# Optimization experiments

Measured on AMD Instinct MI355X. Metric: run time of the kernel, lower is better.

The kernel has to match this reference:

```python
import jax, jax.numpy as jnp
import numpy as np

B, L = 64, 512
CONTACT_P = 0.03  # realistic sparse contact density

def setup_inputs() -> dict:
    key = jax.random.key(0)
    k1, k2, k3 = jax.random.split(key, 3)
    inputs = jax.random.normal(k1, (B, L, L), dtype=jnp.float32)
    targets = (jax.random.uniform(k2, (B, L, L)) < CONTACT_P).astype(jnp.float32)
    seq_lens = jax.random.randint(k3, (B,), 64, L + 1, dtype=jnp.int32)
    return {"inputs": inputs, "targets": targets, "seq_lens": seq_lens}

def reference(inputs, targets, seq_lens):
    # inputs: (B,L,L) logits, targets: (B,L,L) binary, seq_lens: (B,) int
    Bn, Ln, _ = inputs.shape
    ar = jnp.arange(Ln)
    sl = seq_lens[:, None, None]
    mask = ((ar[None, :, None] < sl) & (ar[None, None, :] < sl)).astype(inputs.dtype)  # (B,L,L)

    sl_f = seq_lens.astype(inputs.dtype)
    total_positions = sl_f * sl_f                                  # (B,)
    num_contacts = jnp.sum(targets * mask, axis=(1, 2))            # (B,)
    density = jnp.where(total_positions > 0,
                        num_contacts / jnp.maximum(total_positions, 1.0), 0.0)
    # adaptive weights: computed from .item() in torch => detached constant
    w = jax.lax.stop_gradient(jnp.clip(0.01 / (density + 1e-6), 1.0, 50.0))  # (B,)

    # stable BCE-with-logits with pos_weight w:
    #   loss = w*t*softplus(-x) + (1-t)*(x + softplus(-x))
    sp = jax.nn.softplus(-inputs)
    elem = w[:, None, None] * targets * sp + (1.0 - targets) * (inputs + sp)
    per_sample = jnp.sum(elem * mask, axis=(1, 2)) / jnp.maximum(total_positions, 1.0)
    return jnp.mean(per_sample)
```

## Files before the change

kernel.cpp:

```cpp
#include <hip/hip_runtime.h>
#include <math.h>

#define LDIM 512
#define BDIM 64
#define BLK_PER_S 32
#define ROWSTRIDE (BLK_PER_S*4)

__global__ __launch_bounds__(256) void bce_main_kernel(
    const float* __restrict__ x, const float* __restrict__ t,
    const int* __restrict__ seq_lens, float4* __restrict__ part) {
  const int b = blockIdx.y;
  const int xblk = blockIdx.x;
  const int sl = seq_lens[b];
  const int wave = threadIdx.x >> 6;
  const int lane = threadIdx.x & 63;

  float A = 0.f, P = 0.f, Q = 0.f;
  const int nv = (sl + 3) >> 2;
  const size_t sbase = (size_t)b * LDIM * LDIM;

  for (int i = xblk * 4 + wave; i < sl; i += ROWSTRIDE) {
    const float4* __restrict__ x4 = (const float4*)(x + sbase + (size_t)i * LDIM);
    const float4* __restrict__ t4 = (const float4*)(t + sbase + (size_t)i * LDIM);
    for (int v = lane; v < nv; v += 64) {
      const float4 xv = x4[v];
      const float4 tv = t4[v];
      const float xs[4] = {xv.x, xv.y, xv.z, xv.w};
      const float ts[4] = {tv.x, tv.y, tv.z, tv.w};
      const int j0 = v << 2;
#pragma unroll
      for (int k = 0; k < 4; ++k) {
        const float on = (j0 + k < sl) ? 1.f : 0.f;
        const float xx = xs[k];
        const float tt = ts[k] * on;
        const float ax = fabsf(xx);
        const float m  = __logf(1.f + __expf(-ax));
        const float spn = fmaxf(-xx, 0.f) + m;
        const float spp = fmaxf( xx, 0.f) + m;
        A += tt;
        P += tt * spn;
        Q += (on - tt) * spp;
      }
    }
  }

#pragma unroll
  for (int off = 32; off; off >>= 1) {
    A += __shfl_down(A, off);
    P += __shfl_down(P, off);
    Q += __shfl_down(Q, off);
  }

  __shared__ float s[4][3];
  if (lane == 0) { s[wave][0] = A; s[wave][1] = P; s[wave][2] = Q; }
  __syncthreads();
  if (threadIdx.x == 0) {
    float4 p;
    p.x = s[0][0] + s[1][0] + s[2][0] + s[3][0];
    p.y = s[0][1] + s[1][1] + s[2][1] + s[3][1];
    p.z = s[0][2] + s[1][2] + s[2][2] + s[3][2];
    p.w = 0.f;
    part[b * BLK_PER_S + xblk] = p;
  }
}

__global__ __launch_bounds__(64) void bce_final_kernel(
    const float4* __restrict__ part, const int* __restrict__ seq_lens,
    float* __restrict__ out) {
  const int b = threadIdx.x;
  float A = 0.f, P = 0.f, Q = 0.f;
#pragma unroll
  for (int k = 0; k < BLK_PER_S; ++k) {
    const float4 p = part[b * BLK_PER_S + k];
    A += p.x; P += p.y; Q += p.z;
  }
  const float sl = (float)seq_lens[b];
  const float tp = sl * sl;
  const float density = A / fmaxf(tp, 1.f);
  const float w = fminf(fmaxf(0.01f / (density + 1e-6f), 1.f), 50.f);
  float ps = (w * P + Q) / fmaxf(tp, 1.f);
#pragma unroll
  for (int off = 32; off; off >>= 1) ps += __shfl_down(ps, off);
  if (b == 0) out[0] = ps * (1.f / 64.f);
}

extern "C" void kernel_launch(void* const* d_in, const int* in_sizes, int n_in,
                              void* d_out, int out_size, void* d_ws, size_t ws_size,
                              hipStream_t stream) {
  const float* x = (const float*)d_in[0];
  const float* t = (const float*)d_in[1];
  const int* seq_lens = (const int*)d_in[2];
  float* out = (float*)d_out;
  float4* part = (float4*)d_ws;

  dim3 grid(BLK_PER_S, BDIM);
  bce_main_kernel<<<grid, 256, 0, stream>>>(x, t, seq_lens, part);
  bce_final_kernel<<<1, 64, 0, stream>>>(part, seq_lens, out);
}
```

Baseline: 134.2 us.

## Spread rows across batches per block for load balance, parallelize final reduction

Each wave now owns one row index across four batch samples (strided by 16), so every block gets a mix of short and long sequences instead of all blocks of one sample sharing that sample's length. This balances work across the GPU's compute units despite variable seq_lens. Row loads are issued up front as two fixed float4 pairs per lane to raise memory-level parallelism. The final reduction runs as 64 blocks that combine with atomicAdd into an output zeroed by an added memset, which brings float-atomic ordering nondeterminism and an extra launch.

```diff
diff --git a/kernel.cpp b/kernel.cpp
--- a/kernel.cpp
+++ b/kernel.cpp
@@ -3,85 +3,106 @@
 
 #define LDIM 512
 #define BDIM 64
-#define BLK_PER_S 32
-#define ROWSTRIDE (BLK_PER_S*4)
+#define NBLK 2048
+#define NWAVE (NBLK * 4)
+#define ROWS (BDIM * LDIM)
+#define RPW (ROWS / NWAVE)
+
+__device__ __forceinline__ void accum4(const float4 xv, const float4 tv,
+                                       int j0, int sl,
+                                       float& A, float& P, float& Q) {
+  const float xs[4] = {xv.x, xv.y, xv.z, xv.w};
+  const float ts[4] = {tv.x, tv.y, tv.z, tv.w};
+#pragma unroll
+  for (int k = 0; k < 4; ++k) {
+    const float on = (j0 + k < sl) ? 1.f : 0.f;
+    const float xx = xs[k];
+    const float tt = ts[k] * on;
+    const float ax = fabsf(xx);
+    const float m  = __logf(1.f + __expf(-ax));
+    A += tt;
+    P += tt * (fmaxf(-xx, 0.f) + m);
+    Q += (on - tt) * (fmaxf(xx, 0.f) + m);
+  }
+}
 
 __global__ __launch_bounds__(256) void bce_main_kernel(
     const float* __restrict__ x, const float* __restrict__ t,
-    const int* __restrict__ seq_lens, float4* __restrict__ part) {
-  const int b = blockIdx.y;
-  const int xblk = blockIdx.x;
-  const int sl = seq_lens[b];
+    const int* __restrict__ seq_lens, float* __restrict__ part) {
+  __shared__ int sl_sh[BDIM];
+  __shared__ float psum[4][RPW][3];
   const int wave = threadIdx.x >> 6;
   const int lane = threadIdx.x & 63;
+  if (threadIdx.x < BDIM) sl_sh[threadIdx.x] = seq_lens[threadIdx.x];
+  __syncthreads();
 
-  float A = 0.f, P = 0.f, Q = 0.f;
-  const int nv = (sl + 3) >> 2;
-  const size_t sbase = (size_t)b * LDIM * LDIM;
+  const int gw = blockIdx.x * 4 + wave;
+  const int i  = gw & (LDIM - 1);
+  const int b0 = gw >> 9;
 
-  for (int i = xblk * 4 + wave; i < sl; i += ROWSTRIDE) {
-    const float4* __restrict__ x4 = (const float4*)(x + sbase + (size_t)i * LDIM);
-    const float4* __restrict__ t4 = (const float4*)(t + sbase + (size_t)i * LDIM);
-    for (int v = lane; v < nv; v += 64) {
-      const float4 xv = x4[v];
-      const float4 tv = t4[v];
-      const float xs[4] = {xv.x, xv.y, xv.z, xv.w};
-      const float ts[4] = {tv.x, tv.y, tv.z, tv.w};
-      const int j0 = v << 2;
 #pragma unroll
-      for (int k = 0; k < 4; ++k) {
-        const float on = (j0 + k < sl) ? 1.f : 0.f;
-        const float xx = xs[k];
-        const float tt = ts[k] * on;
-        const float ax = fabsf(xx);
-        const float m  = __logf(1.f + __expf(-ax));
-        const float spn = fmaxf(-xx, 0.f) + m;
-        const float spp = fmaxf( xx, 0.f) + m;
-        A += tt;
-        P += tt * spn;
-        Q += (on - tt) * spp;
+  for (int k = 0; k < RPW; ++k) {
+    const int b  = b0 + 16 * k;
+    const int sl = sl_sh[b];
+    float A = 0.f, P = 0.f, Q = 0.f;
+    if (i < sl) {
+      const size_t base = ((size_t)b * LDIM + (size_t)i) * LDIM;
+      const float4* __restrict__ x4 = (const float4*)(x + base);
+      const float4* __restrict__ t4 = (const float4*)(t + base);
+      const int nv = (sl + 3) >> 2;
+      const int v1 = lane, v2 = lane + 64;
+      const bool h1 = v1 < nv, h2 = v2 < nv;
+      float4 xv1, tv1, xv2, tv2;
+      if (h1) { xv1 = x4[v1]; tv1 = t4[v1]; }
+      if (h2) { xv2 = x4[v2]; tv2 = t4[v2]; }
+      if (h1) accum4(xv1, tv1, v1 << 2, sl, A, P, Q);
+      if (h2) accum4(xv2, tv2, v2 << 2, sl, A, P, Q);
+#pragma unroll
+      for (int off = 32; off; off >>= 1) {
+        A += __shfl_down(A, off);
+        P += __shfl_down(P, off);
+        Q += __shfl_down(Q, off);
       }
     }
+    if (lane == 0) { psum[wave][k][0] = A; psum[wave][k][1] = P; psum[wave][k][2] = Q; }
   }
-
-#pragma unroll
-  for (int off = 32; off; off >>= 1) {
-    A += __shfl_down(A, off);
-    P += __shfl_down(P, off);
-    Q += __shfl_down(Q, off);
-  }
-
-  __shared__ float s[4][3];
-  if (lane == 0) { s[wave][0] = A; s[wave][1] = P; s[wave][2] = Q; }
   __syncthreads();
-  if (threadIdx.x == 0) {
-    float4 p;
-    p.x = s[0][0] + s[1][0] + s[2][0] + s[3][0];
-    p.y = s[0][1] + s[1][1] + s[2][1] + s[3][1];
-    p.z = s[0][2] + s[1][2] + s[2][2] + s[3][2];
-    p.w = 0.f;
-    part[b * BLK_PER_S + xblk] = p;
+  if (threadIdx.x < RPW * 3) {
+    const int k = threadIdx.x / 3, c = threadIdx.x % 3;
+    const float v = psum[0][k][c] + psum[1][k][c] + psum[2][k][c] + psum[3][k][c];
+    part[(size_t)threadIdx.x * NBLK + blockIdx.x] = v;
   }
 }
 
 __global__ __launch_bounds__(64) void bce_final_kernel(
-    const float4* __restrict__ part, const int* __restrict__ seq_lens,
+    const float* __restrict__ part, const int* __restrict__ seq_lens,
     float* __restrict__ out) {
-  const int b = threadIdx.x;
-  float A = 0.f, P = 0.f, Q = 0.f;
+  const int s = blockIdx.x;
+  const int lane = threadIdx.x;
+  const int k = s >> 4, b0 = s & 15;
+  float v0, v1, v2;
+  {
+    const float* p0 = part + (size_t)(k * 3 + 0) * NBLK + b0 * 128;
+    const float* p1 = part + (size_t)(k * 3 + 1) * NBLK + b0 * 128;
+    const float* p2 = part + (size_t)(k * 3 + 2) * NBLK + b0 * 128;
+    v0 = p0[lane] + p0[lane + 64];
+    v1 = p1[lane] + p1[lane + 64];
+    v2 = p2[lane] + p2[lane + 64];
+  }
 #pragma unroll
-  for (int k = 0; k < BLK_PER_S; ++k) {
-    const float4 p = part[b * BLK_PER_S + k];
-    A += p.x; P += p.y; Q += p.z;
+  for (int off = 32; off; off >>= 1) {
+    v0 += __shfl_down(v0, off);
+    v1 += __shfl_down(v1, off);
+    v2 += __shfl_down(v2, off);
   }
-  const float sl = (float)seq_lens[b];
-  const float tp = sl * sl;
-  const float density = A / fmaxf(tp, 1.f);
-  const float w = fminf(fmaxf(0.01f / (density + 1e-6f), 1.f), 50.f);
-  float ps = (w * P + Q) / fmaxf(tp, 1.f);
-#pragma unroll
-  for (int off = 32; off; off >>= 1) ps += __shfl_down(ps, off);
-  if (b == 0) out[0] = ps * (1.f / 64.f);
+  if (lane == 0) {
+    const float sl = (float)seq_lens[s];
+    const float tp = sl * sl;
+    const float density = v0 / fmaxf(tp, 1.f);
+    const float w = fminf(fmaxf(0.01f / (density + 1e-6f), 1.f), 50.f);
+    const float ps = (w * v1 + v2) / fmaxf(tp, 1.f);
+    atomicAdd(out, ps * (1.f / 64.f));
+  }
 }
 
 extern "C" void kernel_launch(void* const* d_in, const int* in_sizes, int n_in,
@@ -91,9 +112,10 @@
   const float* t = (const float*)d_in[1];
   const int* seq_lens = (const int*)d_in[2];
   float* out = (float*)d_out;
-  float4* part = (float4*)d_ws;
+  float* part = (float*)d_ws;
 
-  dim3 grid(BLK_PER_S, BDIM);
-  bce_main_kernel<<<grid, 256, 0, stream>>>(x, t, seq_lens, part);
-  bce_final_kernel<<<1, 64, 0, stream>>>(part, seq_lens, out);
+  hipMemsetAsync(out, 0, sizeof(float), stream);
+
+  bce_main_kernel<<<NBLK, 256, 0, stream>>>(x, t, seq_lens, part);
+  bce_final_kernel<<<BDIM, 64, 0, stream>>>(part, seq_lens, out);
 }
```

After: 138.1 us. 2.9% more time.
